# Performance work log

Measured on AMD Instinct MI355X. Metric: run time of the kernel, lower is better.

The kernel has to match this reference:

```python
import jax, jax.numpy as jnp
import numpy as np

S0, S1 = 256, 256          # spins (up, down)
N = S0 + S1                # total electrons
SINGLE = 256               # single_dim == single_out (residual requires match)
PAIR = 128                 # pair_dim == pair_out
GAIN_TANH = 1.5927812698663017  # ActivationWithGain: 1/std(tanh(N(0,1)))
SQRT2 = 1.4142135623730951


def setup_inputs() -> dict:
    key = jax.random.key(0)
    ks = jax.random.split(key, 7)
    h_one = jax.random.normal(ks[0], (N, SINGLE), jnp.float32)
    h_two = jax.random.normal(ks[1], (N, N, PAIR), jnp.float32)
    din = SINGLE + 2 * PAIR  # one_in feature dim = 512
    # variance_scaling(2, fan_in) kernels; bias ~ Normal(0, sqrt(2))
    W1 = jax.random.normal(ks[2], (din, SINGLE), jnp.float32) * (2.0 / din) ** 0.5
    b1 = jax.random.normal(ks[3], (SINGLE,), jnp.float32) * SQRT2
    Wg = jax.random.normal(ks[4], (2 * SINGLE, SINGLE), jnp.float32) * (2.0 / (2 * SINGLE)) ** 0.5
    W2 = jax.random.normal(ks[5], (PAIR, PAIR), jnp.float32) * (2.0 / PAIR) ** 0.5
    b2 = jax.random.normal(ks[6], (PAIR,), jnp.float32) * SQRT2
    return dict(h_one=h_one, h_two=h_two, W1=W1, b1=b1, Wg=Wg, W2=W2, b2=b2)


def _act(x):
    # ActivationWithGain(tanh): rescale so output variance ~ input variance
    return jnp.tanh(x) * jnp.asarray(GAIN_TANH, x.dtype)


def reference(h_one, h_two, W1, b1, Wg, W2, b2):
    # construct_single_features: per-spin mean of h_two over sender axis
    g2_up = jnp.mean(h_two[:S0], axis=0)            # (N, PAIR)
    g2_dn = jnp.mean(h_two[S0:], axis=0)            # (N, PAIR)
    one_in = jnp.concatenate([h_one, g2_up, g2_dn], axis=1)   # (N, SINGLE+2*PAIR)
    # construct_global_features: per-spin mean of h_one, concat on features
    g1_up = jnp.mean(h_one[:S0], axis=0, keepdims=True)       # (1, SINGLE)
    g1_dn = jnp.mean(h_one[S0:], axis=0, keepdims=True)       # (1, SINGLE)
    global_in = jnp.concatenate([g1_up, g1_dn], axis=-1)      # (1, 2*SINGLE)

    h_one_new = one_in @ W1 + b1 + global_in @ Wg             # (N, SINGLE)
    h_one_new = _act(h_one_new / SQRT2)
    h_one_out = (h_one + h_one_new) / SQRT2                   # residual (shapes match)

    h_two_new = _act(h_two @ W2 + b2)                         # (N, N, PAIR)
    h_two_out = (h_two + h_two_new) / SQRT2                   # residual
    return h_one_out, h_two_out
```

## Files before the change

kernel.cpp:

```cpp
#include <hip/hip_runtime.h>
#include <stdint.h>

#define NN 512
#define PAIR 128
#define SINGLE 256

#define GAINv 1.5927812698663017f
#define RS2 0.70710678118654752f

typedef unsigned int uint;
typedef unsigned short ushort;
typedef short bf16x8 __attribute__((ext_vector_type(8)));
typedef float f32x4 __attribute__((ext_vector_type(4)));

__device__ __forceinline__ ushort f2b(float f){
  union{float f;uint i;}v; v.f=f;
  uint x=v.i;
  return (ushort)((x + 0x7FFFu + ((x>>16)&1u))>>16);
}
__device__ __forceinline__ float tanh_fast(float x){
  float xc = fminf(fmaxf(x,-8.f),8.f);
  float e = __expf(2.f*xc);
  return (e-1.f)*__builtin_amdgcn_rcpf(e+1.f);
}

__global__ __launch_bounds__(256) void k1_prep(const float* __restrict__ h_one,
                                               const float* __restrict__ w2,
                                               float* __restrict__ g1part,
                                               ushort* __restrict__ wt)
{
  const int b = blockIdx.x, t = threadIdx.x;
  if(b < 8){
    const int rb = b*64;
    float s = 0.f;
    for(int i=0;i<64;i++) s += h_one[(size_t)(rb+i)*SINGLE + t];
    g1part[b*SINGLE + t] = s;
  } else {
    const int bb = b-8;
    for(int e=t; e<16*128; e+=256){
      int kl = e>>7, n = e&127;
      int k = bb*16 + kl;
      wt[n*128 + k] = f2b(w2[(size_t)k*128 + n]);
    }
  }
}

__global__ __launch_bounds__(256) void k2_gterm(const float* __restrict__ g1part,
                                                const float* __restrict__ wg,
                                                float* __restrict__ gtermpart)
{
  __shared__ float g1m[512];
  const int t = threadIdx.x;
  g1m[t]     = (g1part[t]      + g1part[256+t]  + g1part[512+t]  + g1part[768+t])  * (1.f/256.f);
  g1m[t+256] = (g1part[1024+t] + g1part[1280+t] + g1part[1536+t] + g1part[1792+t]) * (1.f/256.f);
  __syncthreads();
  const int fb = blockIdx.x*64;
  float s = 0.f;
  for(int f=fb; f<fb+64; f++)
    s += g1m[f]*wg[(size_t)f*SINGLE + t];
  gtermpart[blockIdx.x*SINGLE + t] = s;
}

__global__ __launch_bounds__(256, 3) void k3_htwo(
    const float* __restrict__ h_two,
    const float* __restrict__ b2,
    const ushort* __restrict__ wt,
    float* __restrict__ g2acc,
    float* __restrict__ out_h2)
{
  const int tid  = threadIdx.x;
  const int w    = tid>>6, lane = tid&63;
  const int lq   = lane>>4, lr = lane&15;
  const int spin = blockIdx.x >> 9;
  const int j    = blockIdx.x & 511;

  bf16x8 af[2][4];
  #pragma unroll
  for(int nt=0;nt<2;nt++){
    const int n = w*32 + nt*16 + lr;
    #pragma unroll
    for(int s=0;s<4;s++){
      const int q = (s + w) & 3;
      af[nt][s] = *(const bf16x8*)(wt + n*128 + q*32 + lq*8);
    }
  }
  f32x4 bias[2];
  #pragma unroll
  for(int nt=0;nt<2;nt++){
    const float4 bv = *(const float4*)(b2 + w*32 + nt*16 + lq*4);
    bias[nt] = (f32x4){bv.x, bv.y, bv.z, bv.w};
  }

  const size_t row0 = (size_t)spin*256 + lr;
  const float* rp = h_two + (row0*NN + j)*PAIR;
  float*       op = out_h2 + (row0*NN + j)*PAIR;
  const size_t cstep = (size_t)16*NN*PAIR;

  float g2r[8] = {0.f,0.f,0.f,0.f,0.f,0.f,0.f,0.f};

  #pragma unroll 1
  for(int c=0;c<16;c++){
    const float* rb = rp + (size_t)c*cstep;
    float4 S[8];
    #pragma unroll
    for(int s=0;s<4;s++){
      const int q = (s + w) & 3;
      S[s*2]   = *(const float4*)(rb + q*32 + lq*8);
      S[s*2+1] = *(const float4*)(rb + q*32 + lq*8 + 4);
    }
    const float4 R0 = *(const float4*)(rb + w*32 + lq*4);
    const float4 R1 = *(const float4*)(rb + w*32 + 16 + lq*4);

    g2r[0]+=S[0].x; g2r[1]+=S[0].y; g2r[2]+=S[0].z; g2r[3]+=S[0].w;
    g2r[4]+=S[1].x; g2r[5]+=S[1].y; g2r[6]+=S[1].z; g2r[7]+=S[1].w;

    f32x4 acc0 = bias[0], acc1 = bias[1];
    #pragma unroll
    for(int s=0;s<4;s++){
      bf16x8 bfr;
      const float* sv = (const float*)&S[s*2];
      #pragma unroll
      for(int e=0;e<8;e++) bfr[e] = (short)f2b(sv[e]);
      acc0 = __builtin_amdgcn_mfma_f32_16x16x32_bf16(af[0][s], bfr, acc0, 0,0,0);
      acc1 = __builtin_amdgcn_mfma_f32_16x16x32_bf16(af[1][s], bfr, acc1, 0,0,0);
    }

    float* ob = op + (size_t)c*cstep + w*32 + lq*4;
    f32x4 o0, o1;
    o0[0] = (R0.x + GAINv*tanh_fast(acc0[0]))*RS2;
    o0[1] = (R0.y + GAINv*tanh_fast(acc0[1]))*RS2;
    o0[2] = (R0.z + GAINv*tanh_fast(acc0[2]))*RS2;
    o0[3] = (R0.w + GAINv*tanh_fast(acc0[3]))*RS2;
    o1[0] = (R1.x + GAINv*tanh_fast(acc1[0]))*RS2;
    o1[1] = (R1.y + GAINv*tanh_fast(acc1[1]))*RS2;
    o1[2] = (R1.z + GAINv*tanh_fast(acc1[2]))*RS2;
    o1[3] = (R1.w + GAINv*tanh_fast(acc1[3]))*RS2;
    __builtin_nontemporal_store(o0, (f32x4*)ob);
    __builtin_nontemporal_store(o1, (f32x4*)(ob+16));
  }

  #pragma unroll
  for(int m=1;m<16;m<<=1){
    #pragma unroll
    for(int q=0;q<8;q++) g2r[q] += __shfl_xor(g2r[q], m, 64);
  }
  if(lr < 2){
    f32x4 v;
    if(lr==0){ v[0]=g2r[0]; v[1]=g2r[1]; v[2]=g2r[2]; v[3]=g2r[3]; }
    else     { v[0]=g2r[4]; v[1]=g2r[5]; v[2]=g2r[6]; v[3]=g2r[7]; }
    *(f32x4*)(g2acc + ((size_t)spin*NN + j)*PAIR + w*32 + lq*8 + lr*4) = v;
  }
}

__global__ __launch_bounds__(256) void k4_hone(
    const float* __restrict__ h_one,
    const float* __restrict__ w1,
    const float* __restrict__ b1,
    const float* __restrict__ g2acc,
    const float* __restrict__ gtermpart,
    float* __restrict__ out_h1)
{
  __shared__ float onein[2][512];
  const int n  = threadIdx.x;
  const int r0 = blockIdx.x*2;
  #pragma unroll
  for(int rr=0; rr<2; rr++){
    onein[rr][n] = h_one[(size_t)(r0+rr)*SINGLE + n];
    int sp = n>>7, p = n&127;
    onein[rr][256+n] = g2acc[((size_t)sp*NN + (r0+rr))*PAIR + p] * (1.f/256.f);
  }
  float gt = 0.f;
  #pragma unroll
  for(int bb=0;bb<8;bb++) gt += gtermpart[bb*256+n];
  __syncthreads();
  float a0=0.f, a1=0.f;
  for(int f=0; f<512; f++){
    float wv = w1[(size_t)f*SINGLE + n];
    a0 += onein[0][f]*wv;
    a1 += onein[1][f]*wv;
  }
  const float bn = b1[n];
  float x0 = (a0 + bn + gt)*RS2;
  float x1 = (a1 + bn + gt)*RS2;
  out_h1[(size_t)r0*SINGLE + n]     = (onein[0][n] + GAINv*tanh_fast(x0))*RS2;
  out_h1[(size_t)(r0+1)*SINGLE + n] = (onein[1][n] + GAINv*tanh_fast(x1))*RS2;
}

extern "C" void kernel_launch(void* const* d_in, const int* in_sizes, int n_in,
                              void* d_out, int out_size, void* d_ws, size_t ws_size,
                              hipStream_t stream)
{
  const float* h_one = (const float*)d_in[0];
  const float* h_two = (const float*)d_in[1];
  const float* W1    = (const float*)d_in[2];
  const float* b1    = (const float*)d_in[3];
  const float* Wg    = (const float*)d_in[4];
  const float* W2    = (const float*)d_in[5];
  const float* b2    = (const float*)d_in[6];

  float* wsf       = (float*)d_ws;
  float* g2acc     = wsf;
  ushort* wt       = (ushort*)(wsf + 131072);
  float* g1part    = wsf + 139264;
  float* gtermpart = wsf + 141312;

  float* out_h1 = (float*)d_out;
  float* out_h2 = out_h1 + 131072;

  k1_prep <<<16,   256, 0, stream>>>(h_one, W2, g1part, wt);
  k2_gterm<<<8,    256, 0, stream>>>(g1part, Wg, gtermpart);
  k3_htwo <<<1024, 256, 0, stream>>>(h_two, b2, wt, g2acc, out_h2);
  k4_hone <<<256,  256, 0, stream>>>(h_one, W1, b1, g2acc, gtermpart, out_h1);
}
```

Baseline: 340.0 us.

## Stage h_two tiles in swizzled LDS as bf16 and accumulate g2 via atomics

The h_two kernel now gives each block a 16x4 (i,j) tile. It loads the tile once with coalesced float4 reads, converts it to bf16 into XOR-swizzled shared memory, and runs MFMA over four M-tiles per wave. The per-spin sender sum is computed from the shared tile and combined across blocks with global atomicAdd into a buffer that k1_prep now zeroes. The block count grows fourfold and launch bounds ask for higher occupancy. The residual is re-read from global memory, and the per-spin mean is now summed from bf16-rounded values instead of fp32, which reduces its accuracy.

```diff
diff --git a/kernel.cpp b/kernel.cpp
--- a/kernel.cpp
+++ b/kernel.cpp
@@ -18,6 +18,8 @@
   uint x=v.i;
   return (ushort)((x + 0x7FFFu + ((x>>16)&1u))>>16);
 }
+__device__ __forceinline__ float b2f_lo(uint u){ union{uint i;float f;}v; v.i=u<<16; return v.f; }
+__device__ __forceinline__ float b2f_hi(uint u){ union{uint i;float f;}v; v.i=u&0xFFFF0000u; return v.f; }
 __device__ __forceinline__ float tanh_fast(float x){
   float xc = fminf(fmaxf(x,-8.f),8.f);
   float e = __expf(2.f*xc);
@@ -27,7 +29,8 @@
 __global__ __launch_bounds__(256) void k1_prep(const float* __restrict__ h_one,
                                                const float* __restrict__ w2,
                                                float* __restrict__ g1part,
-                                               ushort* __restrict__ wt)
+                                               ushort* __restrict__ wt,
+                                               float* __restrict__ g2acc)
 {
   const int b = blockIdx.x, t = threadIdx.x;
   if(b < 8){
@@ -35,13 +38,17 @@
     float s = 0.f;
     for(int i=0;i<64;i++) s += h_one[(size_t)(rb+i)*SINGLE + t];
     g1part[b*SINGLE + t] = s;
-  } else {
+  } else if(b < 16){
     const int bb = b-8;
     for(int e=t; e<16*128; e+=256){
       int kl = e>>7, n = e&127;
       int k = bb*16 + kl;
       wt[n*128 + k] = f2b(w2[(size_t)k*128 + n]);
     }
+  } else {
+    f32x4 z = (f32x4){0.f,0.f,0.f,0.f};
+    f32x4* dst = (f32x4*)g2acc + (size_t)(b-16)*4096;
+    for(int q=t; q<4096; q+=256) dst[q] = z;
   }
 }
 
@@ -61,28 +68,38 @@
   gtermpart[blockIdx.x*SINGLE + t] = s;
 }
 
-__global__ __launch_bounds__(256, 3) void k3_htwo(
+__global__ __launch_bounds__(256, 4) void k3_htwo(
     const float* __restrict__ h_two,
     const float* __restrict__ b2,
     const ushort* __restrict__ wt,
     float* __restrict__ g2acc,
     float* __restrict__ out_h2)
 {
-  const int tid  = threadIdx.x;
-  const int w    = tid>>6, lane = tid&63;
-  const int lq   = lane>>4, lr = lane&15;
-  const int spin = blockIdx.x >> 9;
-  const int j    = blockIdx.x & 511;
+  __shared__ __align__(16) ushort At[64*128];
+  const int tid = threadIdx.x;
+  const int w = tid>>6, lane = tid&63;
+  const int lq = lane>>4, lr = lane&15;
+  const int bi = blockIdx.x & 31, bj = blockIdx.x >> 5;
+  const int i0 = bi*16, j0 = bj*4;
+  const int spin = bi>>4;
+
+  #pragma unroll
+  for(int rep=0;rep<8;rep++){
+    const int e = rep*1024 + tid*4;
+    const int di = e>>9, c = e&511;
+    const float4 v = *(const float4*)(h_two + ((size_t)(i0+di)*NN + j0)*PAIR + c);
+    ushort4 pk; pk.x=f2b(v.x); pk.y=f2b(v.y); pk.z=f2b(v.z); pk.w=f2b(v.w);
+    const int r = e>>7;
+    *(ushort4*)(&At[e ^ ((r&7)<<3)]) = pk;
+  }
 
   bf16x8 af[2][4];
   #pragma unroll
   for(int nt=0;nt<2;nt++){
     const int n = w*32 + nt*16 + lr;
     #pragma unroll
-    for(int s=0;s<4;s++){
-      const int q = (s + w) & 3;
-      af[nt][s] = *(const bf16x8*)(wt + n*128 + q*32 + lq*8);
-    }
+    for(int kk=0;kk<4;kk++)
+      af[nt][kk] = *(const bf16x8*)(wt + n*128 + kk*32 + lq*8);
   }
   f32x4 bias[2];
   #pragma unroll
@@ -90,65 +107,59 @@
     const float4 bv = *(const float4*)(b2 + w*32 + nt*16 + lq*4);
     bias[nt] = (f32x4){bv.x, bv.y, bv.z, bv.w};
   }
-
-  const size_t row0 = (size_t)spin*256 + lr;
-  const float* rp = h_two + (row0*NN + j)*PAIR;
-  float*       op = out_h2 + (row0*NN + j)*PAIR;
-  const size_t cstep = (size_t)16*NN*PAIR;
-
-  float g2r[8] = {0.f,0.f,0.f,0.f,0.f,0.f,0.f,0.f};
-
-  #pragma unroll 1
-  for(int c=0;c<16;c++){
-    const float* rb = rp + (size_t)c*cstep;
-    float4 S[8];
-    #pragma unroll
-    for(int s=0;s<4;s++){
-      const int q = (s + w) & 3;
-      S[s*2]   = *(const float4*)(rb + q*32 + lq*8);
-      S[s*2+1] = *(const float4*)(rb + q*32 + lq*8 + 4);
-    }
-    const float4 R0 = *(const float4*)(rb + w*32 + lq*4);
-    const float4 R1 = *(const float4*)(rb + w*32 + 16 + lq*4);
-
-    g2r[0]+=S[0].x; g2r[1]+=S[0].y; g2r[2]+=S[0].z; g2r[3]+=S[0].w;
-    g2r[4]+=S[1].x; g2r[5]+=S[1].y; g2r[6]+=S[1].z; g2r[7]+=S[1].w;
-
-    f32x4 acc0 = bias[0], acc1 = bias[1];
-    #pragma unroll
-    for(int s=0;s<4;s++){
-      bf16x8 bfr;
-      const float* sv = (const float*)&S[s*2];
-      #pragma unroll
-      for(int e=0;e<8;e++) bfr[e] = (short)f2b(sv[e]);
-      acc0 = __builtin_amdgcn_mfma_f32_16x16x32_bf16(af[0][s], bfr, acc0, 0,0,0);
-      acc1 = __builtin_amdgcn_mfma_f32_16x16x32_bf16(af[1][s], bfr, acc1, 0,0,0);
-    }
-
-    float* ob = op + (size_t)c*cstep + w*32 + lq*4;
-    f32x4 o0, o1;
-    o0[0] = (R0.x + GAINv*tanh_fast(acc0[0]))*RS2;
-    o0[1] = (R0.y + GAINv*tanh_fast(acc0[1]))*RS2;
-    o0[2] = (R0.z + GAINv*tanh_fast(acc0[2]))*RS2;
-    o0[3] = (R0.w + GAINv*tanh_fast(acc0[3]))*RS2;
-    o1[0] = (R1.x + GAINv*tanh_fast(acc1[0]))*RS2;
-    o1[1] = (R1.y + GAINv*tanh_fast(acc1[1]))*RS2;
-    o1[2] = (R1.z + GAINv*tanh_fast(acc1[2]))*RS2;
-    o1[3] = (R1.w + GAINv*tanh_fast(acc1[3]))*RS2;
-    __builtin_nontemporal_store(o0, (f32x4*)ob);
-    __builtin_nontemporal_store(o1, (f32x4*)(ob+16));
-  }
-
-  #pragma unroll
-  for(int m=1;m<16;m<<=1){
-    #pragma unroll
-    for(int q=0;q<8;q++) g2r[q] += __shfl_xor(g2r[q], m, 64);
-  }
-  if(lr < 2){
-    f32x4 v;
-    if(lr==0){ v[0]=g2r[0]; v[1]=g2r[1]; v[2]=g2r[2]; v[3]=g2r[3]; }
-    else     { v[0]=g2r[4]; v[1]=g2r[5]; v[2]=g2r[6]; v[3]=g2r[7]; }
-    *(f32x4*)(g2acc + ((size_t)spin*NN + j)*PAIR + w*32 + lq*8 + lr*4) = v;
+  __syncthreads();
+
+  {
+    const int dj = w, pp = lane;
+    const uint* a32 = (const uint*)At;
+    float s0=0.f, s1=0.f;
+    #pragma unroll
+    for(int di=0;di<16;di++){
+      const int r = di*4+dj;
+      uint u = a32[(r*64 + pp) ^ ((r&7)<<2)];
+      s0 += b2f_lo(u); s1 += b2f_hi(u);
+    }
+    float* dst = g2acc + ((size_t)spin*NN + (j0+dj))*PAIR + pp*2;
+    atomicAdd(dst, s0); atomicAdd(dst+1, s1);
+  }
+
+  f32x4 acc[4][2];
+  #pragma unroll
+  for(int mt=0;mt<4;mt++){
+    acc[mt][0] = bias[0];
+    acc[mt][1] = bias[1];
+  }
+  #pragma unroll
+  for(int kk=0;kk<4;kk++){
+    bf16x8 bfr[4];
+    #pragma unroll
+    for(int mt=0;mt<4;mt++){
+      const int m = mt*16 + lr;
+      const int e = m*128 + kk*32 + lq*8;
+      bfr[mt] = *(const bf16x8*)(&At[e ^ ((lr&7)<<3)]);
+    }
+    #pragma unroll
+    for(int mt=0;mt<4;mt++){
+      acc[mt][0] = __builtin_amdgcn_mfma_f32_16x16x32_bf16(af[0][kk], bfr[mt], acc[mt][0], 0,0,0);
+      acc[mt][1] = __builtin_amdgcn_mfma_f32_16x16x32_bf16(af[1][kk], bfr[mt], acc[mt][1], 0,0,0);
+    }
+  }
+
+  #pragma unroll
+  for(int mt=0;mt<4;mt++){
+    const int m = mt*16 + lr;
+    const size_t base = ((size_t)(i0 + (m>>2))*NN + (j0 + (m&3)))*PAIR;
+    #pragma unroll
+    for(int nt=0;nt<2;nt++){
+      const int nb = w*32 + nt*16 + lq*4;
+      const float4 rr = *(const float4*)(h_two + base + nb);
+      f32x4 o;
+      o[0] = (rr.x + GAINv*tanh_fast(acc[mt][nt][0]))*RS2;
+      o[1] = (rr.y + GAINv*tanh_fast(acc[mt][nt][1]))*RS2;
+      o[2] = (rr.z + GAINv*tanh_fast(acc[mt][nt][2]))*RS2;
+      o[3] = (rr.w + GAINv*tanh_fast(acc[mt][nt][3]))*RS2;
+      *(f32x4*)(out_h2 + base + nb) = o;
+    }
   }
 }
 
@@ -207,8 +218,8 @@
   float* out_h1 = (float*)d_out;
   float* out_h2 = out_h1 + 131072;
 
-  k1_prep <<<16,   256, 0, stream>>>(h_one, W2, g1part, wt);
+  k1_prep <<<24,   256, 0, stream>>>(h_one, W2, g1part, wt, g2acc);
   k2_gterm<<<8,    256, 0, stream>>>(g1part, Wg, gtermpart);
-  k3_htwo <<<1024, 256, 0, stream>>>(h_two, b2, wt, g2acc, out_h2);
+  k3_htwo <<<4096, 256, 0, stream>>>(h_two, b2, wt, g2acc, out_h2);
   k4_hone <<<256,  256, 0, stream>>>(h_one, W1, b1, g2acc, gtermpart, out_h1);
 }
```

Result: faster. 314.7 us (-7.5%).
